# Kernel optimization log

Measured on AMD Instinct MI355X. Metric: run time of the kernel, lower is better.

The kernel has to match this reference:

```python
import jax, jax.numpy as jnp
import numpy as np

CUTOFF = 5.0
LOG2 = float(np.log(2.0))

def ssp(u):
    # shifted softplus: softplus(x) - log(2)
    return jax.nn.softplus(u) - LOG2

def setup_inputs() -> dict:
    key = jax.random.key(0)
    ks = jax.random.split(key, 12)
    B, A, Nn, F, S = 8, 1024, 64, 128, 64
    x = jax.random.normal(ks[0], (B, A, F), jnp.float32)
    r_ij = jax.random.uniform(ks[1], (B, A, Nn), jnp.float32)
    f_ij = jax.random.normal(ks[2], (B, A, Nn, S), jnp.float32)
    neighbors = jax.random.randint(ks[3], (B, A, Nn), 0, A)
    neighbor_mask = jax.random.randint(ks[4], (B, A, Nn), 0, 2).astype(bool)
    # parameters (xavier-ish scale)
    W_in2f = jax.random.normal(ks[5], (F, F), jnp.float32) / np.sqrt(F)   # in2f: no bias
    W1 = jax.random.normal(ks[6], (S, F), jnp.float32) / np.sqrt(S)
    b1 = jnp.zeros((F,), jnp.float32)
    W2 = jax.random.normal(ks[7], (F, F), jnp.float32) / np.sqrt(F)
    b2 = jnp.zeros((F,), jnp.float32)
    W_f2out = jax.random.normal(ks[8], (F, F), jnp.float32) / np.sqrt(F)
    b_f2out = jnp.zeros((F,), jnp.float32)
    W_dense = jax.random.normal(ks[9], (F, F), jnp.float32) / np.sqrt(F)
    b_dense = jnp.zeros((F,), jnp.float32)
    return dict(x=x, r_ij=r_ij, f_ij=f_ij, neighbors=neighbors,
                neighbor_mask=neighbor_mask, W_in2f=W_in2f, W1=W1, b1=b1,
                W2=W2, b2=b2, W_f2out=W_f2out, b_f2out=b_f2out,
                W_dense=W_dense, b_dense=b_dense)

def reference(x, r_ij, f_ij, neighbors, neighbor_mask,
              W_in2f, W1, b1, W2, b2, W_f2out, b_f2out, W_dense, b_dense):
    # filter-generating network on expanded distances: (B,A,Nn,S) -> (B,A,Nn,F)
    W = ssp(jnp.einsum('bans,sf->banf', f_ij, W1) + b1)
    W = jnp.einsum('banf,fg->bang', W, W2) + b2
    # hard cutoff mask
    C = (r_ij <= CUTOFF).astype(x.dtype)          # (B,A,Nn)
    W = W * C[..., None]
    # project atom features and gather neighbor features
    y = jnp.einsum('baf,fg->bag', x, W_in2f)       # (B,A,F)
    nbh = jax.vmap(lambda yb, ib: yb[ib])(y, neighbors)  # (B,A,Nn,F)
    # continuous-filter convolution + masked sum over neighbors
    agg = jnp.sum(nbh * W * neighbor_mask[..., None].astype(x.dtype), axis=2)  # (B,A,F)
    v = ssp(jnp.einsum('baf,fg->bag', agg, W_f2out) + b_f2out)
    # final interaction dense (no activation)
    out = jnp.einsum('baf,fg->bag', v, W_dense) + b_dense
    return out
```

## Files before the change

### kernel.cpp

```cpp
#include <hip/hip_runtime.h>
#include <math.h>

#define NB 8
#define NA 1024
#define NN 64
#define NF 128
#define NS 64
#define LN2 0.69314718055994530942f
#define HSTR 136

typedef __attribute__((ext_vector_type(8))) short bf16x8;
typedef __attribute__((ext_vector_type(4))) float f32x4;
typedef __attribute__((ext_vector_type(4))) unsigned u32x4;

__device__ __forceinline__ float ssp(float x) {
    return fmaxf(x, 0.0f) + __logf(1.0f + __expf(-fabsf(x))) - LN2;
}
__device__ __forceinline__ short f2bf(float f) {
    unsigned u = __float_as_uint(f);
    u += 0x7fffu + ((u >> 16) & 1u);
    return (short)(u >> 16);
}
__device__ __forceinline__ unsigned pkbf(float a, float b) {
    unsigned r;
    asm("v_cvt_pk_bf16_f32 %0, %1, %2" : "=v"(r) : "v"(a), "v"(b));
    return r;
}
__device__ __forceinline__ float bf2f(short s) {
    return __uint_as_float(((unsigned)(unsigned short)s) << 16);
}

__device__ __forceinline__ void swz_frag(const float* __restrict__ W, short* __restrict__ Wf, int t) {
    int k = t >> 7, n = t & 127;
    int kt = k >> 5, lg = (k >> 3) & 3, j = k & 7, ntg = n >> 4, col = n & 15;
    Wf[((kt * 8 + ntg) * 64 + (lg * 16 + col)) * 8 + j] = f2bf(W[t]);
}

__global__ __launch_bounds__(256) void k_prep(const float* __restrict__ W1,
                                              const float* __restrict__ W2,
                                              const float* __restrict__ Winf,
                                              const float* __restrict__ Wf2,
                                              const float* __restrict__ Wd,
                                              short* __restrict__ W1f, short* __restrict__ W2f,
                                              short* __restrict__ Winff, short* __restrict__ Wf2f,
                                              short* __restrict__ Wdf) {
    int t = blockIdx.x * 256 + threadIdx.x;
    if (t < NS * NF) swz_frag(W1, W1f, t);
    swz_frag(W2, W2f, t);
    swz_frag(Winf, Winff, t);
    swz_frag(Wf2, Wf2f, t);
    swz_frag(Wd, Wdf, t);
}

__device__ __forceinline__ void stage32(const float* __restrict__ src, char* __restrict__ dst, int t) {
    int row = t >> 3, seg = t & 7;
    const float4* sp = (const float4*)(src + (size_t)row * NF + seg * 16);
    float4 a = sp[0], b = sp[1], c = sp[2], d = sp[3];
    u32x4 lo = (u32x4){pkbf(a.x, a.y), pkbf(a.z, a.w), pkbf(b.x, b.y), pkbf(b.z, b.w)};
    u32x4 hi = (u32x4){pkbf(c.x, c.y), pkbf(c.z, c.w), pkbf(d.x, d.y), pkbf(d.z, d.w)};
    int base = row * 256 + seg * 32;
    int sw = (row & 7) << 4;
    *(u32x4*)(dst + ((base) ^ sw))      = lo;
    *(u32x4*)(dst + ((base + 16) ^ sw)) = hi;
}

__global__ __launch_bounds__(256) void k_in2f_m(const float* __restrict__ x,
                                                const short* __restrict__ Wf,
                                                float* __restrict__ y) {
    __shared__ __align__(16) char xL[32 * 256];
    int t = threadIdx.x, lane = t & 63, wid = t >> 6;
    int row0 = blockIdx.x * 32;

    stage32(x + (size_t)row0 * NF, xL, t);
    __syncthreads();

    int rowA = lane & 15, kgrp = lane >> 4, goff = wid * 32;
    f32x4 acc[2][2];
#pragma unroll
    for (int mt = 0; mt < 2; mt++) {
        acc[mt][0] = (f32x4){0.f, 0.f, 0.f, 0.f};
        acc[mt][1] = (f32x4){0.f, 0.f, 0.f, 0.f};
    }
#pragma unroll
    for (int kt = 0; kt < 4; kt++) {
        bf16x8 bf0 = *(const bf16x8*)&Wf[((kt * 8 + wid * 2 + 0) * 64 + lane) * 8];
        bf16x8 bf1 = *(const bf16x8*)&Wf[((kt * 8 + wid * 2 + 1) * 64 + lane) * 8];
#pragma unroll
        for (int mt = 0; mt < 2; mt++) {
            int row = mt * 16 + rowA;
            int byte = (row * 256 + kt * 64 + kgrp * 16) ^ ((row & 7) << 4);
            bf16x8 af = *(const bf16x8*)(xL + byte);
            acc[mt][0] = __builtin_amdgcn_mfma_f32_16x16x32_bf16(af, bf0, acc[mt][0], 0, 0, 0);
            acc[mt][1] = __builtin_amdgcn_mfma_f32_16x16x32_bf16(af, bf1, acc[mt][1], 0, 0, 0);
        }
    }
#pragma unroll
    for (int mt = 0; mt < 2; mt++)
#pragma unroll
        for (int nt = 0; nt < 2; nt++)
#pragma unroll
            for (int r = 0; r < 4; r++)
                y[(size_t)(row0 + mt * 16 + kgrp * 4 + r) * NF + goff + nt * 16 + (lane & 15)] = acc[mt][nt][r];
}

__global__ __launch_bounds__(256) void k_out_m(float* buf,
                                               const short* __restrict__ Wf2f, const float* __restrict__ bf2,
                                               const short* __restrict__ Wdf, const float* __restrict__ bd) {
    __shared__ __align__(16) char xL[32 * 256];
    __shared__ short vL[32 * HSTR];
    int t = threadIdx.x, lane = t & 63, wid = t >> 6;
    int row0 = blockIdx.x * 32;

    stage32(buf + (size_t)row0 * NF, xL, t);
    __syncthreads();

    int rowA = lane & 15, kgrp = lane >> 4, goff = wid * 32;
    int gc0 = goff + (lane & 15), gc1 = gc0 + 16;
    float bb0 = bf2[gc0], bb1 = bf2[gc1];

    f32x4 acc[2][2];
#pragma unroll
    for (int mt = 0; mt < 2; mt++) {
        acc[mt][0] = (f32x4){bb0, bb0, bb0, bb0};
        acc[mt][1] = (f32x4){bb1, bb1, bb1, bb1};
    }
#pragma unroll
    for (int kt = 0; kt < 4; kt++) {
        bf16x8 bf0 = *(const bf16x8*)&Wf2f[((kt * 8 + wid * 2 + 0) * 64 + lane) * 8];
        bf16x8 bf1 = *(const bf16x8*)&Wf2f[((kt * 8 + wid * 2 + 1) * 64 + lane) * 8];
#pragma unroll
        for (int mt = 0; mt < 2; mt++) {
            int row = mt * 16 + rowA;
            int byte = (row * 256 + kt * 64 + kgrp * 16) ^ ((row & 7) << 4);
            bf16x8 af = *(const bf16x8*)(xL + byte);
            acc[mt][0] = __builtin_amdgcn_mfma_f32_16x16x32_bf16(af, bf0, acc[mt][0], 0, 0, 0);
            acc[mt][1] = __builtin_amdgcn_mfma_f32_16x16x32_bf16(af, bf1, acc[mt][1], 0, 0, 0);
        }
    }
#pragma unroll
    for (int mt = 0; mt < 2; mt++)
#pragma unroll
        for (int nt = 0; nt < 2; nt++) {
            int col = goff + nt * 16 + (lane & 15);
            int r0 = mt * 16 + kgrp * 4;
            unsigned p01 = pkbf(ssp(acc[mt][nt][0]), ssp(acc[mt][nt][1]));
            unsigned p23 = pkbf(ssp(acc[mt][nt][2]), ssp(acc[mt][nt][3]));
            vL[(r0 + 0) * HSTR + col] = (short)(p01 & 0xffffu);
            vL[(r0 + 1) * HSTR + col] = (short)(p01 >> 16);
            vL[(r0 + 2) * HSTR + col] = (short)(p23 & 0xffffu);
            vL[(r0 + 3) * HSTR + col] = (short)(p23 >> 16);
        }
    __syncthreads();

    float bd0 = bd[gc0], bd1 = bd[gc1];
    f32x4 acc2[2][2];
#pragma unroll
    for (int mt = 0; mt < 2; mt++) {
        acc2[mt][0] = (f32x4){bd0, bd0, bd0, bd0};
        acc2[mt][1] = (f32x4){bd1, bd1, bd1, bd1};
    }
#pragma unroll
    for (int kt = 0; kt < 4; kt++) {
        bf16x8 bf0 = *(const bf16x8*)&Wdf[((kt * 8 + wid * 2 + 0) * 64 + lane) * 8];
        bf16x8 bf1 = *(const bf16x8*)&Wdf[((kt * 8 + wid * 2 + 1) * 64 + lane) * 8];
#pragma unroll
        for (int mt = 0; mt < 2; mt++) {
            bf16x8 af = *(const bf16x8*)&vL[(mt * 16 + rowA) * HSTR + kt * 32 + kgrp * 8];
            acc2[mt][0] = __builtin_amdgcn_mfma_f32_16x16x32_bf16(af, bf0, acc2[mt][0], 0, 0, 0);
            acc2[mt][1] = __builtin_amdgcn_mfma_f32_16x16x32_bf16(af, bf1, acc2[mt][1], 0, 0, 0);
        }
    }
#pragma unroll
    for (int mt = 0; mt < 2; mt++)
#pragma unroll
        for (int nt = 0; nt < 2; nt++)
#pragma unroll
            for (int r = 0; r < 4; r++)
                buf[(size_t)(row0 + mt * 16 + kgrp * 4 + r) * NF + goff + nt * 16 + (lane & 15)] = acc2[mt][nt][r];
}

__global__ __launch_bounds__(256) void k_conv(
        const float* __restrict__ fij, const float* __restrict__ rij,
        const int* __restrict__ nbr, const int* __restrict__ nmask,
        const float* __restrict__ y,
        const short* __restrict__ W1f, const float* __restrict__ b1,
        const short* __restrict__ W2f, const float* __restrict__ b2,
        float* __restrict__ agg) {
    __shared__ __align__(16) char smem[8192 + NN * HSTR * 2];
    __shared__ int cOff[NN];
    __shared__ float2 red2[4][NF / 2];

    short* hL  = (short*)(smem + 8192);
    short* wfB = (short*)smem;

    int t = threadIdx.x;
    int ba = blockIdx.x;
    int b = ba >> 10;
    int lane = t & 63;
    int wid = t >> 6;

    const float* fsrc = fij + (size_t)ba * NN * NS;

    unsigned long long bal;
    {
        float r = rij[(size_t)ba * NN + lane];
        int mk = nmask[(size_t)ba * NN + lane];
        bool valid = (mk != 0) && (r <= 5.0f);
        bal = __ballot(valid);
        if (wid == 0 && valid) {
            int pos = __popcll(bal & ((1ULL << lane) - 1ULL));
            cOff[pos] = nbr[(size_t)ba * NN + lane] << 7;
        }
    }
    int V = (int)__popcll(bal);
    int MT = (V + 15) >> 4;

    {
        int n = t >> 2;
        if ((bal >> n) & 1ULL) {
            int pos = __popcll(bal & ((1ULL << n) - 1ULL));
            int k0 = (t & 3) * 16;
            const float4* src = (const float4*)(fsrc + (size_t)n * NS + k0);
            float4 a = src[0], bb = src[1], c = src[2], d = src[3];
            u32x4 lo = (u32x4){pkbf(a.x, a.y), pkbf(a.z, a.w), pkbf(bb.x, bb.y), pkbf(bb.z, bb.w)};
            u32x4 hi = (u32x4){pkbf(c.x, c.y), pkbf(c.z, c.w), pkbf(d.x, d.y), pkbf(d.z, d.w)};
            int base = pos * 128 + k0 * 2;
            int sw = (pos & 7) << 4;
            *(u32x4*)(smem + ((base) ^ sw))      = lo;
            *(u32x4*)(smem + ((base + 16) ^ sw)) = hi;
        }
    }
    __syncthreads();

    int rowA = lane & 15;
    int kgrp = lane >> 4;
    int goff = wid * 32;

    int gc0 = goff + (lane & 15);
    int gc1 = gc0 + 16;
    float b1v0 = b1[gc0], b1v1 = b1[gc1];
    float b2v0 = b2[gc0], b2v1 = b2[gc1];

    f32x4 acc[4][2];
#pragma unroll
    for (int mt = 0; mt < 4; mt++) {
        acc[mt][0] = (f32x4){b1v0, b1v0, b1v0, b1v0};
        acc[mt][1] = (f32x4){b1v1, b1v1, b1v1, b1v1};
    }
#pragma unroll
    for (int kt = 0; kt < 2; kt++) {
        bf16x8 bf0 = *(const bf16x8*)&W1f[((kt * 8 + wid * 2 + 0) * 64 + lane) * 8];
        bf16x8 bf1 = *(const bf16x8*)&W1f[((kt * 8 + wid * 2 + 1) * 64 + lane) * 8];
#pragma unroll
        for (int mt = 0; mt < 4; mt++) {
            if (mt < MT) {
                int row = mt * 16 + rowA;
                int byte = (row * 128 + kt * 64 + kgrp * 16) ^ ((row & 7) << 4);
                bf16x8 af = *(const bf16x8*)(smem + byte);
                acc[mt][0] = __builtin_amdgcn_mfma_f32_16x16x32_bf16(af, bf0, acc[mt][0], 0, 0, 0);
                acc[mt][1] = __builtin_amdgcn_mfma_f32_16x16x32_bf16(af, bf1, acc[mt][1], 0, 0, 0);
            }
        }
    }

#pragma unroll
    for (int mt = 0; mt < 4; mt++) {
        if (mt < MT) {
#pragma unroll
            for (int nt = 0; nt < 2; nt++) {
                int col = goff + nt * 16 + (lane & 15);
                int row0 = mt * 16 + kgrp * 4;
                unsigned p01 = pkbf(ssp(acc[mt][nt][0]), ssp(acc[mt][nt][1]));
                unsigned p23 = pkbf(ssp(acc[mt][nt][2]), ssp(acc[mt][nt][3]));
                hL[(row0 + 0) * HSTR + col] = (short)(p01 & 0xffffu);
                hL[(row0 + 1) * HSTR + col] = (short)(p01 >> 16);
                hL[(row0 + 2) * HSTR + col] = (short)(p23 & 0xffffu);
                hL[(row0 + 3) * HSTR + col] = (short)(p23 >> 16);
            }
        }
    }
    __syncthreads();

    f32x4 acc2[4][2];
#pragma unroll
    for (int mt = 0; mt < 4; mt++) {
        acc2[mt][0] = (f32x4){b2v0, b2v0, b2v0, b2v0};
        acc2[mt][1] = (f32x4){b2v1, b2v1, b2v1, b2v1};
    }
#pragma unroll
    for (int kt = 0; kt < 4; kt++) {
        bf16x8 bf0 = *(const bf16x8*)&W2f[((kt * 8 + wid * 2 + 0) * 64 + lane) * 8];
        bf16x8 bf1 = *(const bf16x8*)&W2f[((kt * 8 + wid * 2 + 1) * 64 + lane) * 8];
#pragma unroll
        for (int mt = 0; mt < 4; mt++) {
            if (mt < MT) {
                bf16x8 af = *(const bf16x8*)&hL[(mt * 16 + rowA) * HSTR + kt * 32 + kgrp * 8];
                acc2[mt][0] = __builtin_amdgcn_mfma_f32_16x16x32_bf16(af, bf0, acc2[mt][0], 0, 0, 0);
                acc2[mt][1] = __builtin_amdgcn_mfma_f32_16x16x32_bf16(af, bf1, acc2[mt][1], 0, 0, 0);
            }
        }
    }
    __syncthreads();

#pragma unroll
    for (int mt = 0; mt < 4; mt++) {
        if (mt < MT) {
#pragma unroll
            for (int nt = 0; nt < 2; nt++) {
                int col = goff + nt * 16 + (lane & 15);
                int row0 = mt * 16 + kgrp * 4;
                unsigned p01 = pkbf(acc2[mt][nt][0], acc2[mt][nt][1]);
                unsigned p23 = pkbf(acc2[mt][nt][2], acc2[mt][nt][3]);
                wfB[(row0 + 0) * HSTR + col] = (short)(p01 & 0xffffu);
                wfB[(row0 + 1) * HSTR + col] = (short)(p01 >> 16);
                wfB[(row0 + 2) * HSTR + col] = (short)(p23 & 0xffffu);
                wfB[(row0 + 3) * HSTR + col] = (short)(p23 >> 16);
            }
        }
    }
    __syncthreads();

    int gp = t & 63;
    int sl = t >> 6;
    int g2 = gp * 2;
    const float* yb = y + (size_t)b * NA * NF;
    float lx = 0.0f, ly = 0.0f;
#pragma unroll 4
    for (int j = sl; j < V; j += 4) {
        unsigned wv2 = *(const unsigned*)&wfB[j * HSTR + g2];
        float2 yv = *(const float2*)&yb[(size_t)cOff[j] + g2];
        lx = fmaf(yv.x, bf2f((short)(wv2 & 0xffffu)), lx);
        ly = fmaf(yv.y, bf2f((short)(wv2 >> 16)), ly);
    }
    red2[sl][gp] = (float2){lx, ly};
    __syncthreads();
    if (t < 64) {
        float2 a0 = red2[0][t], a1 = red2[1][t], a2 = red2[2][t], a3 = red2[3][t];
        float2 s;
        s.x = (a0.x + a1.x) + (a2.x + a3.x);
        s.y = (a0.y + a1.y) + (a2.y + a3.y);
        *(float2*)&agg[(size_t)ba * NF + t * 2] = s;
    }
}

extern "C" void kernel_launch(void* const* d_in, const int* in_sizes, int n_in,
                              void* d_out, int out_size, void* d_ws, size_t ws_size,
                              hipStream_t stream) {
    const float* x    = (const float*)d_in[0];
    const float* rij  = (const float*)d_in[1];
    const float* fij  = (const float*)d_in[2];
    const int*   nbr  = (const int*)d_in[3];
    const int*   nmask = (const int*)d_in[4];
    const float* W_in2f = (const float*)d_in[5];
    const float* W1   = (const float*)d_in[6];
    const float* b1   = (const float*)d_in[7];
    const float* W2   = (const float*)d_in[8];
    const float* b2   = (const float*)d_in[9];
    const float* Wf2  = (const float*)d_in[10];
    const float* bf2  = (const float*)d_in[11];
    const float* Wd   = (const float*)d_in[12];
    const float* bd   = (const float*)d_in[13];

    float* out = (float*)d_out;
    float* y   = (float*)d_ws;
    short* W1f   = (short*)((char*)d_ws + (size_t)NB * NA * NF * 4);
    short* W2f   = W1f + NS * NF;
    short* Winff = W2f + NF * NF;
    short* Wf2f  = Winff + NF * NF;
    short* Wdf   = Wf2f + NF * NF;

    const int rows = NB * NA;

    k_prep<<<64, 256, 0, stream>>>(W1, W2, W_in2f, Wf2, Wd, W1f, W2f, Winff, Wf2f, Wdf);
    k_in2f_m<<<rows / 32, 256, 0, stream>>>(x, Winff, y);
    k_conv<<<rows, 256, 0, stream>>>(fij, rij, nbr, nmask, y, W1f, b1, W2f, b2, out);
    k_out_m<<<rows / 32, 256, 0, stream>>>(out, Wf2f, bf2, Wdf, bd);
}
```

Baseline: 71.90 us.

## Store filter tile transposed and give each wave its own feature columns in aggregation

The filter matrix is now written to shared memory transposed (feature-major, stride JSTR) with packed 64-bit stores instead of four scalar 16-bit stores. In the gather-aggregate phase each lane pair owns one feature column and walks neighbors in groups of 8, combining the two halves with a lane shuffle. This removes the shared-memory cross-wave reduction and its extra barrier. In exchange, the y gathers become scalar 4-byte loads per neighbor rather than float2, and padded neighbors are zero-filled in cOff.

Measured after the change: 76.71 us. 6.7% more time.

```diff
diff --git a/kernel.cpp b/kernel.cpp
--- a/kernel.cpp
+++ b/kernel.cpp
@@ -8,10 +8,12 @@
 #define NS 64
 #define LN2 0.69314718055994530942f
 #define HSTR 136
+#define JSTR 72
 
 typedef __attribute__((ext_vector_type(8))) short bf16x8;
 typedef __attribute__((ext_vector_type(4))) float f32x4;
 typedef __attribute__((ext_vector_type(4))) unsigned u32x4;
+typedef __attribute__((ext_vector_type(2))) unsigned u32x2;
 
 __device__ __forceinline__ float ssp(float x) {
     return fmaxf(x, 0.0f) + __logf(1.0f + __expf(-fabsf(x))) - LN2;
@@ -188,10 +190,9 @@
         float* __restrict__ agg) {
     __shared__ __align__(16) char smem[8192 + NN * HSTR * 2];
     __shared__ int cOff[NN];
-    __shared__ float2 red2[4][NF / 2];
 
     short* hL  = (short*)(smem + 8192);
-    short* wfB = (short*)smem;
+    short* wfT = (short*)smem;
 
     int t = threadIdx.x;
     int ba = blockIdx.x;
@@ -207,9 +208,13 @@
         int mk = nmask[(size_t)ba * NN + lane];
         bool valid = (mk != 0) && (r <= 5.0f);
         bal = __ballot(valid);
-        if (wid == 0 && valid) {
-            int pos = __popcll(bal & ((1ULL << lane) - 1ULL));
-            cOff[pos] = nbr[(size_t)ba * NN + lane] << 7;
+        if (wid == 0) {
+            if (valid) {
+                int pos = __popcll(bal & ((1ULL << lane) - 1ULL));
+                cOff[pos] = nbr[(size_t)ba * NN + lane] << 7;
+            }
+            int V0 = (int)__popcll(bal);
+            if (lane >= V0) cOff[lane] = 0;
         }
     }
     int V = (int)__popcll(bal);
@@ -308,39 +313,33 @@
 #pragma unroll
             for (int nt = 0; nt < 2; nt++) {
                 int col = goff + nt * 16 + (lane & 15);
-                int row0 = mt * 16 + kgrp * 4;
-                unsigned p01 = pkbf(acc2[mt][nt][0], acc2[mt][nt][1]);
-                unsigned p23 = pkbf(acc2[mt][nt][2], acc2[mt][nt][3]);
-                wfB[(row0 + 0) * HSTR + col] = (short)(p01 & 0xffffu);
-                wfB[(row0 + 1) * HSTR + col] = (short)(p01 >> 16);
-                wfB[(row0 + 2) * HSTR + col] = (short)(p23 & 0xffffu);
-                wfB[(row0 + 3) * HSTR + col] = (short)(p23 >> 16);
-            }
-        }
-    }
-    __syncthreads();
-
-    int gp = t & 63;
-    int sl = t >> 6;
-    int g2 = gp * 2;
+                int r0 = mt * 16 + kgrp * 4;
+                u32x2 pk = (u32x2){pkbf(acc2[mt][nt][0], acc2[mt][nt][1]),
+                                   pkbf(acc2[mt][nt][2], acc2[mt][nt][3])};
+                *(u32x2*)&wfT[col * JSTR + r0] = pk;
+            }
+        }
+    }
+    __syncthreads();
+
+    int g = goff + (lane >> 1);
+    int half = lane & 1;
     const float* yb = y + (size_t)b * NA * NF;
-    float lx = 0.0f, ly = 0.0f;
-#pragma unroll 4
-    for (int j = sl; j < V; j += 4) {
-        unsigned wv2 = *(const unsigned*)&wfB[j * HSTR + g2];
-        float2 yv = *(const float2*)&yb[(size_t)cOff[j] + g2];
-        lx = fmaf(yv.x, bf2f((short)(wv2 & 0xffffu)), lx);
-        ly = fmaf(yv.y, bf2f((short)(wv2 >> 16)), ly);
-    }
-    red2[sl][gp] = (float2){lx, ly};
-    __syncthreads();
-    if (t < 64) {
-        float2 a0 = red2[0][t], a1 = red2[1][t], a2 = red2[2][t], a3 = red2[3][t];
-        float2 s;
-        s.x = (a0.x + a1.x) + (a2.x + a3.x);
-        s.y = (a0.y + a1.y) + (a2.y + a3.y);
-        *(float2*)&agg[(size_t)ba * NF + t * 2] = s;
-    }
+    float p = 0.0f;
+    int Vp8 = (V + 7) >> 3;
+    for (int jb = half; jb < Vp8; jb += 2) {
+        int j0 = jb * 8;
+        u32x4 wv = *(const u32x4*)&wfT[g * JSTR + j0];
+#pragma unroll
+        for (int e = 0; e < 8; e++) {
+            int j = j0 + e;
+            unsigned w16 = (e & 1) ? (wv[e >> 1] >> 16) : (wv[e >> 1] & 0xffffu);
+            float wf = (j < V) ? bf2f((short)w16) : 0.0f;
+            p = fmaf(yb[(size_t)cOff[j] + g], wf, p);
+        }
+    }
+    p += __shfl_xor(p, 1, 64);
+    if (half == 0) agg[(size_t)ba * NF + g] = p;
 }
 
 extern "C" void kernel_launch(void* const* d_in, const int* in_sizes, int n_in,
```
